# Kernel tuning notes

Measured on AMD Instinct MI355X. Metric: run time of the kernel, lower is better.

## Reference

```python
import jax, jax.numpy as jnp
import numpy as np

N_HEADS = 16
ROPE_BASE = 10000.0


def _rope(x):
    # x: (B, T, H, D) -> rotary position embedding, half-split style
    T, D = x.shape[1], x.shape[-1]
    inv_freq = 1.0 / (ROPE_BASE ** (jnp.arange(0, D, 2, dtype=jnp.float32) / D))  # (D/2,)
    ang = jnp.arange(T, dtype=jnp.float32)[:, None] * inv_freq[None, :]            # (T, D/2)
    cos = jnp.cos(ang)[None, :, None, :].astype(x.dtype)
    sin = jnp.sin(ang)[None, :, None, :].astype(x.dtype)
    x1, x2 = jnp.split(x, 2, axis=-1)
    return jnp.concatenate([x1 * cos - x2 * sin, x2 * cos + x1 * sin], axis=-1)


def setup_inputs() -> dict:
    key = jax.random.key(0)
    k1, k2, k3 = jax.random.split(key, 3)
    B, T, C = 4, 2048, 2048
    init_std = 0.02
    n_layers = 24  # n_text_layers + n_vision_layers
    x = jax.random.normal(k1, (B, T, C), dtype=jnp.float32)
    Wqkv = jax.random.normal(k2, (C, 3 * C), dtype=jnp.float32) * init_std
    Wproj = jax.random.normal(k3, (C, C), dtype=jnp.float32) * (init_std * 2 * n_layers ** (-0.5))
    return {"x": x, "Wqkv": Wqkv, "Wproj": Wproj}


def reference(x, Wqkv, Wproj):
    B, T, C = x.shape
    D = C // N_HEADS
    qkv = x @ Wqkv                                  # (B, T, 3C) fused QKV projection
    q, k, v = jnp.split(qkv, 3, axis=-1)
    q = q.reshape(B, T, N_HEADS, D)
    k = k.reshape(B, T, N_HEADS, D)
    v = v.reshape(B, T, N_HEADS, D)
    q = _rope(q)
    k = _rope(k)
    y = jax.nn.dot_product_attention(q, k, v, is_causal=True)  # (B, T, H, D)
    y = y.reshape(B, T, C)
    return y @ Wproj
```

## Files before the change

kernel.cpp:

```cpp
#include <hip/hip_runtime.h>

#define BB 4
#define TT 2048
#define CC 2048
#define NHEAD 16
#define DH 128
#define MM (BB * TT)
#define N3 (3 * CC)
#define LD3 6144

typedef unsigned short u16;
typedef __attribute__((ext_vector_type(8))) short short8;
typedef __attribute__((ext_vector_type(4))) float f32x4;

__device__ __forceinline__ u16 f2bf(float f) {
  unsigned u = __float_as_uint(f);
  u += 0x7fffu + ((u >> 16) & 1u);
  return (u16)(u >> 16);
}
__device__ __forceinline__ float bf2f(u16 h) {
  return __uint_as_float(((unsigned)h) << 16);
}

__device__ __forceinline__ void gload_lds16(const void* g, void* l) {
  __builtin_amdgcn_global_load_lds((const __attribute__((address_space(1))) void*)g,
                                   (__attribute__((address_space(3))) void*)l, 16, 0, 0);
}

__device__ __forceinline__ f32x4 mfma16(short8 a, short8 b, f32x4 c) {
  return __builtin_amdgcn_mfma_f32_16x16x32_bf16(a, b, c, 0, 0, 0);
}

__global__ void convert_x_kernel(const float* __restrict__ x, u16* __restrict__ xb) {
  const int total = (MM * CC) / 4;
  const float4* xv = (const float4*)x;
  ushort4* ov = (ushort4*)xb;
  for (int i = blockIdx.x * blockDim.x + threadIdx.x; i < total; i += gridDim.x * blockDim.x) {
    float4 v = xv[i];
    ushort4 o;
    o.x = f2bf(v.x); o.y = f2bf(v.y); o.z = f2bf(v.z); o.w = f2bf(v.w);
    ov[i] = o;
  }
}

__global__ void transpose_bf16_kernel(const float* __restrict__ W, u16* __restrict__ Wt,
                                      int rows, int cols) {
  __shared__ float tile[32][33];
  const int n0 = blockIdx.x * 32, k0 = blockIdx.y * 32;
  const int tx = threadIdx.x, ty = threadIdx.y;
  #pragma unroll
  for (int i = 0; i < 4; ++i)
    tile[ty + 8 * i][tx] = W[(size_t)(k0 + ty + 8 * i) * cols + n0 + tx];
  __syncthreads();
  #pragma unroll
  for (int i = 0; i < 4; ++i)
    Wt[(size_t)(n0 + ty + 8 * i) * rows + k0 + tx] = f2bf(tile[tx][ty + 8 * i]);
}

__global__ void rope_table_kernel(float2* __restrict__ tab) {
  int idx = blockIdx.x * 256 + threadIdx.x;
  int t = idx >> 6, f = idx & 63;
  float freq = expf(-0.14391156831f * (float)f);
  float ang = (float)t * freq;
  float s, c;
  sincosf(ang, &s, &c);
  tab[idx] = make_float2(c, s);
}

__global__ void rope_apply_kernel(u16* __restrict__ qkv, const float2* __restrict__ tab) {
  int idx = blockIdx.x * 256 + threadIdx.x;
  int f8 = idx & 7;
  int h = (idx >> 3) & 15;
  int m = (idx >> 7) & 8191;
  int which = idx >> 20;
  int t = m & (TT - 1);
  u16* p = qkv + (size_t)m * LD3 + which * CC + h * DH + f8 * 8;
  short8 v1 = *(const short8*)p;
  short8 v2 = *(const short8*)(p + 64);
  const float2* cs = &tab[(t << 6) + f8 * 8];
  const float scale = which ? 1.0f : 0.08838834764831845f;
  short8 o1, o2;
  #pragma unroll
  for (int j = 0; j < 8; ++j) {
    float2 c = cs[j];
    float x1 = bf2f((u16)v1[j]), x2 = bf2f((u16)v2[j]);
    o1[j] = (short)f2bf((x1 * c.x - x2 * c.y) * scale);
    o2[j] = (short)f2bf((x2 * c.x + x1 * c.y) * scale);
  }
  *(short8*)p = o1;
  *(short8*)(p + 64) = o2;
}

#define TILE_B 32768

__device__ __forceinline__ int swz47(int x) { return x ^ (((x >> 7) & 7) << 4); }

__device__ __forceinline__ void stage_chunk(const u16* __restrict__ src, int K, int k0,
                                            char* ldsTile, int kind, int wid, int lane) {
  #pragma unroll
  for (int c = 0; c < 2; ++c) {
    int x;
    if (kind < 2) {
      x = (kind ? 8192 : 0) + c * 16384 + wid * 1024 + lane * 16;
    } else {
      int wl = wid * 2 + c;
      x = ((kind == 3) ? 4096 : 0) + (wl >> 2) * 8192 + (wl & 3) * 1024 + lane * 16;
    }
    int l = swz47(x);
    int r = l >> 7;
    int ce = (l >> 1) & 63;
    gload_lds16(src + (size_t)r * K + k0 + ce, ldsTile + (x - lane * 16));
  }
}

__global__ __launch_bounds__(512, 2) void gemm_bt_256(const u16* __restrict__ A,
                                                      const u16* __restrict__ Bt,
                                                      void* __restrict__ Cout,
                                                      int K, int ldc, int out_bf16) {
  __shared__ __align__(16) char As[2][TILE_B];
  __shared__ __align__(16) char Bs[2][TILE_B];
  const int tid = threadIdx.x;
  const int wid = tid >> 6, lane = tid & 63;
  const int l15 = lane & 15, g = lane >> 4;
  const int wr = wid >> 2, wc = wid & 3;
  const int nwg = gridDim.x * gridDim.y;
  const int orig = blockIdx.y * gridDim.x + blockIdx.x;
  const int swz = (orig & 7) * (nwg >> 3) + (orig >> 3);
  const int bx = swz % gridDim.x, by = swz / gridDim.x;
  const int row0 = by * 256, col0 = bx * 256;

  const u16* Ab = A + (size_t)row0 * K;
  const u16* Bb = Bt + (size_t)col0 * K;

  f32x4 acc[8][4];
  #pragma unroll
  for (int m = 0; m < 8; ++m)
    #pragma unroll
    for (int n = 0; n < 4; ++n) acc[m][n] = (f32x4){0.f, 0.f, 0.f, 0.f};

  const int abase = (wr * 128 + l15) * 128 + g * 16;
  const int bbase = (wc * 64 + l15) * 128 + g * 16;

  stage_chunk(Ab, K, 0, As[0], 0, wid, lane);
  stage_chunk(Bb, K, 0, Bs[0], 2, wid, lane);
  stage_chunk(Bb, K, 0, Bs[0], 3, wid, lane);
  stage_chunk(Ab, K, 0, As[0], 1, wid, lane);
  asm volatile("s_waitcnt vmcnt(0)" ::: "memory");
  __builtin_amdgcn_s_barrier();

  const int nt = K >> 6;
  short8 a[4][2], blo[2][2], bhi[2][2];
  for (int kt = 0; kt < nt; ++kt) {
    const int cur = kt & 1, nx = cur ^ 1;
    const bool hn = (kt + 1) < nt;
    const int kn = (kt + 1) << 6;
    const char* At = As[cur];
    const char* Btl = Bs[cur];

    #pragma unroll
    for (int m = 0; m < 4; ++m)
      #pragma unroll
      for (int ks = 0; ks < 2; ++ks)
        a[m][ks] = *(const short8*)(At + swz47(abase + m * 2048 + ks * 64));
    #pragma unroll
    for (int n = 0; n < 2; ++n)
      #pragma unroll
      for (int ks = 0; ks < 2; ++ks)
        blo[n][ks] = *(const short8*)(Btl + swz47(bbase + n * 2048 + ks * 64));
    if (hn) stage_chunk(Ab, K, kn, As[nx], 0, wid, lane);
    __builtin_amdgcn_s_barrier();
    __builtin_amdgcn_s_setprio(1);
    #pragma unroll
    for (int m = 0; m < 4; ++m)
      #pragma unroll
      for (int n = 0; n < 2; ++n)
        #pragma unroll
        for (int ks = 0; ks < 2; ++ks)
          acc[m][n] = mfma16(a[m][ks], blo[n][ks], acc[m][n]);
    __builtin_amdgcn_s_setprio(0);
    if (hn) asm volatile("s_waitcnt vmcnt(4)" ::: "memory");
    else    asm volatile("s_waitcnt vmcnt(2)" ::: "memory");
    __builtin_amdgcn_s_barrier();

    #pragma unroll
    for (int n = 0; n < 2; ++n)
      #pragma unroll
      for (int ks = 0; ks < 2; ++ks)
        bhi[n][ks] = *(const short8*)(Btl + swz47(bbase + (n + 2) * 2048 + ks * 64));
    if (hn) stage_chunk(Bb, K, kn, Bs[nx], 2, wid, lane);
    __builtin_amdgcn_s_barrier();
    __builtin_amdgcn_s_setprio(1);
    #pragma unroll
    for (int m = 0; m < 4; ++m)
      #pragma unroll
      for (int n = 0; n < 2; ++n)
        #pragma unroll
        for (int ks = 0; ks < 2; ++ks)
          acc[m][n + 2] = mfma16(a[m][ks], bhi[n][ks], acc[m][n + 2]);
    __builtin_amdgcn_s_setprio(0);
    if (hn) asm volatile("s_waitcnt vmcnt(4)" ::: "memory");
    else    asm volatile("s_waitcnt vmcnt(0)" ::: "memory");
    __builtin_amdgcn_s_barrier();

    #pragma unroll
    for (int m = 0; m < 4; ++m)
      #pragma unroll
      for (int ks = 0; ks < 2; ++ks)
        a[m][ks] = *(const short8*)(At + swz47(abase + (m + 4) * 2048 + ks * 64));
    if (hn) stage_chunk(Bb, K, kn, Bs[nx], 3, wid, lane);
    __builtin_amdgcn_s_barrier();
    __builtin_amdgcn_s_setprio(1);
    #pragma unroll
    for (int m = 0; m < 4; ++m)
      #pragma unroll
      for (int n = 0; n < 2; ++n)
        #pragma unroll
        for (int ks = 0; ks < 2; ++ks)
          acc[m + 4][n] = mfma16(a[m][ks], blo[n][ks], acc[m + 4][n]);
    __builtin_amdgcn_s_setprio(0);
    if (hn) asm volatile("s_waitcnt vmcnt(4)" ::: "memory");
    __builtin_amdgcn_s_barrier();

    if (hn) stage_chunk(Ab, K, kn, As[nx], 1, wid, lane);
    __builtin_amdgcn_s_barrier();
    __builtin_amdgcn_s_setprio(1);
    #pragma unroll
    for (int m = 0; m < 4; ++m)
      #pragma unroll
      for (int n = 0; n < 2; ++n)
        #pragma unroll
        for (int ks = 0; ks < 2; ++ks)
          acc[m + 4][n + 2] = mfma16(a[m][ks], bhi[n][ks], acc[m + 4][n + 2]);
    __builtin_amdgcn_s_setprio(0);
    if (hn) asm volatile("s_waitcnt vmcnt(4)" ::: "memory");
    __builtin_amdgcn_s_barrier();
  }

  if (out_bf16) {
    u16* Cb = (u16*)Cout;
    #pragma unroll
    for (int m = 0; m < 8; ++m)
      #pragma unroll
      for (int n = 0; n < 4; ++n) {
        int row = row0 + wr * 128 + m * 16 + 4 * g;
        int col = col0 + wc * 64 + n * 16 + l15;
        #pragma unroll
        for (int j = 0; j < 4; ++j)
          Cb[(size_t)(row + j) * ldc + col] = f2bf(acc[m][n][j]);
      }
  } else {
    float* Cf = (float*)Cout;
    #pragma unroll
    for (int m = 0; m < 8; ++m)
      #pragma unroll
      for (int n = 0; n < 4; ++n) {
        int row = row0 + wr * 128 + m * 16 + 4 * g;
        int col = col0 + wc * 64 + n * 16 + l15;
        #pragma unroll
        for (int j = 0; j < 4; ++j)
          Cf[(size_t)(row + j) * ldc + col] = acc[m][n][j];
      }
  }
}

#define QBLK 128
#define KBLK 64
#define PADV 72

__global__ __launch_bounds__(256, 2) void attn_kernel(const u16* __restrict__ qkv,
                                                      u16* __restrict__ y) {
  __shared__ __align__(16) u16 Ks[2][KBLK * 128];
  __shared__ __align__(16) u16 Vt[2][DH * PADV];
  const int tid = threadIdx.x;
  const int wid = tid >> 6, lane = tid & 63;
  const int l15 = lane & 15, g = lane >> 4;
  const int b = blockIdx.y >> 4, h = blockIdx.y & 15;
  const size_t rb = (size_t)b * TT;
  const int vk0 = (tid & 15) * 4, vd0 = (tid >> 4) * 8;

  for (int half = 0; half < 2; ++half) {
    const int qt0 = (half ? (15 - (int)blockIdx.x) : (int)blockIdx.x) * QBLK;

    short8 qf[2][4];
    {
      const u16* qbase = qkv + (rb + qt0 + wid * 32 + l15) * LD3 + h * DH;
      #pragma unroll
      for (int f = 0; f < 2; ++f)
        #pragma unroll
        for (int kk = 0; kk < 4; ++kk)
          qf[f][kk] = *(const short8*)(qbase + f * 16 * LD3 + kk * 32 + g * 8);
    }

    {
      const u16* kbase = qkv + (rb)*LD3 + CC + h * DH;
      #pragma unroll
      for (int c = 0; c < 4; ++c) {
        int chunk = c * 256 + tid;
        int r = chunk >> 4, s = chunk & 15;
        gload_lds16(kbase + (size_t)r * LD3 + (size_t)((s ^ (r & 7)) * 8),
                    &Ks[0][(c * 256 + wid * 64) * 8]);
      }
      const u16* vg = qkv + (rb + vk0) * LD3 + 2 * CC + h * DH + vd0;
      short8 r0 = *(const short8*)vg;
      short8 r1 = *(const short8*)(vg + LD3);
      short8 r2 = *(const short8*)(vg + 2 * LD3);
      short8 r3 = *(const short8*)(vg + 3 * LD3);
      #pragma unroll
      for (int j = 0; j < 8; ++j) {
        ushort4 w;
        w.x = (u16)r0[j]; w.y = (u16)r1[j]; w.z = (u16)r2[j]; w.w = (u16)r3[j];
        *(ushort4*)&Vt[0][(vd0 + j) * PADV + vk0] = w;
      }
    }
    asm volatile("s_waitcnt vmcnt(0)" ::: "memory");
    __syncthreads();

    f32x4 o[2][8];
    float mrun[2][4], lrun[2][4];
    #pragma unroll
    for (int f = 0; f < 2; ++f) {
      #pragma unroll
      for (int nf = 0; nf < 8; ++nf) o[f][nf] = (f32x4){0.f, 0.f, 0.f, 0.f};
      #pragma unroll
      for (int j = 0; j < 4; ++j) { mrun[f][j] = -1e30f; lrun[f][j] = 0.f; }
    }

    const int nt = qt0 / KBLK + 2;
    for (int it = 0; it < nt; ++it) {
      const int cur = it & 1, nxt = cur ^ 1;
      const bool havenext = (it + 1) < nt;
      if (havenext) {
        const int kvn = (it + 1) * KBLK;
        const u16* kbase = qkv + (rb + kvn) * LD3 + CC + h * DH;
        #pragma unroll
        for (int c = 0; c < 4; ++c) {
          int chunk = c * 256 + tid;
          int r = chunk >> 4, s = chunk & 15;
          gload_lds16(kbase + (size_t)r * LD3 + (size_t)((s ^ (r & 7)) * 8),
                      &Ks[nxt][(c * 256 + wid * 64) * 8]);
        }
      }

      f32x4 s4[2][4];
      #pragma unroll
      for (int f = 0; f < 2; ++f)
        #pragma unroll
        for (int jf = 0; jf < 4; ++jf) s4[f][jf] = (f32x4){0.f, 0.f, 0.f, 0.f};
      #pragma unroll
      for (int jf = 0; jf < 4; ++jf) {
        int krow = jf * 16 + l15;
        #pragma unroll
        for (int kk = 0; kk < 4; ++kk) {
          short8 kf = *(const short8*)((const char*)Ks[cur] + krow * 256 +
                                       ((kk * 64 + g * 16) ^ ((l15 & 7) << 4)));
          s4[0][jf] = mfma16(qf[0][kk], kf, s4[0][jf]);
          s4[1][jf] = mfma16(qf[1][kk], kf, s4[1][jf]);
        }
      }
      if (it >= nt - 2) {
        const int kvb = it * KBLK - qt0;
        #pragma unroll
        for (int f = 0; f < 2; ++f)
          #pragma unroll
          for (int jf = 0; jf < 4; ++jf)
            #pragma unroll
            for (int j = 0; j < 4; ++j)
              if (kvb + jf * 16 + l15 > wid * 32 + f * 16 + 4 * g + j)
                s4[f][jf][j] = -1e30f;
      }
      {
        float rmax[2][4];
        #pragma unroll
        for (int f = 0; f < 2; ++f) {
          #pragma unroll
          for (int j = 0; j < 4; ++j)
            rmax[f][j] = fmaxf(fmaxf(s4[f][0][j], s4[f][1][j]),
                               fmaxf(s4[f][2][j], s4[f][3][j]));
          #pragma unroll
          for (int j = 0; j < 4; ++j) {
            rmax[f][j] = fmaxf(rmax[f][j], __shfl_xor(rmax[f][j], 1, 64));
            rmax[f][j] = fmaxf(rmax[f][j], __shfl_xor(rmax[f][j], 2, 64));
            rmax[f][j] = fmaxf(rmax[f][j], __shfl_xor(rmax[f][j], 4, 64));
            rmax[f][j] = fmaxf(rmax[f][j], __shfl_xor(rmax[f][j], 8, 64));
          }
        }
        bool small = true;
        #pragma unroll
        for (int f = 0; f < 2; ++f)
          #pragma unroll
          for (int j = 0; j < 4; ++j)
            small = small && (rmax[f][j] <= mrun[f][j] + 8.0f);
        if (!__all((int)small)) {
          #pragma unroll
          for (int f = 0; f < 2; ++f)
            #pragma unroll
            for (int j = 0; j < 4; ++j) {
              float mn = fmaxf(mrun[f][j], rmax[f][j]);
              float corr = __expf(mrun[f][j] - mn);
              mrun[f][j] = mn;
              lrun[f][j] *= corr;
              #pragma unroll
              for (int nf = 0; nf < 8; ++nf) o[f][nf][j] *= corr;
            }
        }
        #pragma unroll
        for (int f = 0; f < 2; ++f) {
          float rsum[4];
          #pragma unroll
          for (int jf = 0; jf < 4; ++jf)
            #pragma unroll
            for (int j = 0; j < 4; ++j)
              s4[f][jf][j] = __expf(s4[f][jf][j] - mrun[f][j]);
          #pragma unroll
          for (int j = 0; j < 4; ++j) {
            rsum[j] = (s4[f][0][j] + s4[f][1][j]) + (s4[f][2][j] + s4[f][3][j]);
            rsum[j] += __shfl_xor(rsum[j], 1, 64);
            rsum[j] += __shfl_xor(rsum[j], 2, 64);
            rsum[j] += __shfl_xor(rsum[j], 4, 64);
            rsum[j] += __shfl_xor(rsum[j], 8, 64);
            lrun[f][j] += rsum[j];
          }
        }
      }

      __syncthreads();
      {
        u16* Pb = (u16*)Ks[cur];
        #pragma unroll
        for (int f = 0; f < 2; ++f)
          #pragma unroll
          for (int jf = 0; jf < 4; ++jf)
            #pragma unroll
            for (int j = 0; j < 4; ++j) {
              int prow = wid * 32 + f * 16 + 4 * g + j;
              int pcol = (jf * 16 + l15) ^ (((4 * g + j) & 7) << 3);
              Pb[prow * 64 + pcol] = f2bf(s4[f][jf][j]);
            }
      }
      asm volatile("s_waitcnt lgkmcnt(0)" ::: "memory");
      __builtin_amdgcn_sched_barrier(0);
      short8 pf[2][2];
      #pragma unroll
      for (int f = 0; f < 2; ++f)
        #pragma unroll
        for (int kk = 0; kk < 2; ++kk)
          pf[f][kk] = *(const short8*)&((const u16*)Ks[cur])[
              (wid * 32 + f * 16 + l15) * 64 + ((kk * 32 + g * 8) ^ ((l15 & 7) << 3))];

      #pragma unroll
      for (int nf = 0; nf < 8; ++nf) {
        #pragma unroll
        for (int kk = 0; kk < 2; ++kk) {
          short8 vf = *(const short8*)&Vt[cur][(nf * 16 + l15) * PADV + kk * 32 + g * 8];
          o[0][nf] = mfma16(pf[0][kk], vf, o[0][nf]);
          o[1][nf] = mfma16(pf[1][kk], vf, o[1][nf]);
        }
      }

      if (havenext) {
        const int kvn = (it + 1) * KBLK;
        const u16* vg = qkv + (rb + kvn + vk0) * LD3 + 2 * CC + h * DH + vd0;
        short8 r0 = *(const short8*)vg;
        short8 r1 = *(const short8*)(vg + LD3);
        short8 r2 = *(const short8*)(vg + 2 * LD3);
        short8 r3 = *(const short8*)(vg + 3 * LD3);
        #pragma unroll
        for (int j = 0; j < 8; ++j) {
          ushort4 w;
          w.x = (u16)r0[j]; w.y = (u16)r1[j]; w.z = (u16)r2[j]; w.w = (u16)r3[j];
          *(ushort4*)&Vt[nxt][(vd0 + j) * PADV + vk0] = w;
        }
      }
      asm volatile("s_waitcnt vmcnt(0)" ::: "memory");
      __syncthreads();
    }

    #pragma unroll
    for (int f = 0; f < 2; ++f) {
      float inv[4];
      #pragma unroll
      for (int j = 0; j < 4; ++j) inv[j] = 1.0f / lrun[f][j];
      #pragma unroll
      for (int nf = 0; nf < 8; ++nf)
        #pragma unroll
        for (int j = 0; j < 4; ++j)
          y[(rb + qt0 + wid * 32 + f * 16 + 4 * g + j) * CC + h * DH + nf * 16 + l15] =
              f2bf(o[f][nf][j] * inv[j]);
    }
  }
}

extern "C" void kernel_launch(void* const* d_in, const int* in_sizes, int n_in,
                              void* d_out, int out_size, void* d_ws, size_t ws_size,
                              hipStream_t stream) {
  const float* x = (const float*)d_in[0];
  const float* Wqkv = (const float*)d_in[1];
  const float* Wproj = (const float*)d_in[2];
  char* ws = (char*)d_ws;
  u16* xb     = (u16*)(ws);
  u16* wqkvT  = (u16*)(ws + 33554432);
  u16* wprojT = (u16*)(ws + 58720256);
  u16* qkv    = (u16*)(ws + 67108864);
  u16* y      = (u16*)(ws + 167772160);
  float2* tab = (float2*)(ws + 201326592);

  convert_x_kernel<<<4096, 256, 0, stream>>>(x, xb);
  transpose_bf16_kernel<<<dim3(192, 64), dim3(32, 8), 0, stream>>>(Wqkv, wqkvT, CC, N3);
  transpose_bf16_kernel<<<dim3(64, 64), dim3(32, 8), 0, stream>>>(Wproj, wprojT, CC, CC);
  rope_table_kernel<<<512, 256, 0, stream>>>(tab);
  gemm_bt_256<<<dim3(24, 32), 512, 0, stream>>>(xb, wqkvT, (void*)qkv, CC, LD3, 1);
  rope_apply_kernel<<<8192, 256, 0, stream>>>(qkv, tab);
  attn_kernel<<<dim3(8, 64), 256, 0, stream>>>(qkv, y);
  gemm_bt_256<<<dim3(8, 32), 512, 0, stream>>>(y, wprojT, d_out, CC, CC, 0);
}
```

Baseline: 495.3 us.

## Fuse RoPE and query scaling into the QKV GEMM epilogue

Removes the separate rope_apply kernel and applies rotary embedding plus the query softmax scale directly in the QKV GEMM's bf16 store. To make this possible, the B-column assignment across waves is remapped so each wave holds both halves (d and d+64) of a head in registers. This saves a full read-modify-write pass over the Q and K parts of the qkv buffer. In exchange, the epilogue does per-element table lookups with strided scalar stores, and the changed column mapping may alter LDS access patterns.

Result: faster. 479.9 us (-3.1%).

```diff
diff --git a/kernel.cpp b/kernel.cpp
--- a/kernel.cpp
+++ b/kernel.cpp
@@ -67,30 +67,6 @@
   tab[idx] = make_float2(c, s);
 }
 
-__global__ void rope_apply_kernel(u16* __restrict__ qkv, const float2* __restrict__ tab) {
-  int idx = blockIdx.x * 256 + threadIdx.x;
-  int f8 = idx & 7;
-  int h = (idx >> 3) & 15;
-  int m = (idx >> 7) & 8191;
-  int which = idx >> 20;
-  int t = m & (TT - 1);
-  u16* p = qkv + (size_t)m * LD3 + which * CC + h * DH + f8 * 8;
-  short8 v1 = *(const short8*)p;
-  short8 v2 = *(const short8*)(p + 64);
-  const float2* cs = &tab[(t << 6) + f8 * 8];
-  const float scale = which ? 1.0f : 0.08838834764831845f;
-  short8 o1, o2;
-  #pragma unroll
-  for (int j = 0; j < 8; ++j) {
-    float2 c = cs[j];
-    float x1 = bf2f((u16)v1[j]), x2 = bf2f((u16)v2[j]);
-    o1[j] = (short)f2bf((x1 * c.x - x2 * c.y) * scale);
-    o2[j] = (short)f2bf((x2 * c.x + x1 * c.y) * scale);
-  }
-  *(short8*)p = o1;
-  *(short8*)(p + 64) = o2;
-}
-
 #define TILE_B 32768
 
 __device__ __forceinline__ int swz47(int x) { return x ^ (((x >> 7) & 7) << 4); }
@@ -116,7 +92,9 @@
 __global__ __launch_bounds__(512, 2) void gemm_bt_256(const u16* __restrict__ A,
                                                       const u16* __restrict__ Bt,
                                                       void* __restrict__ Cout,
-                                                      int K, int ldc, int out_bf16) {
+                                                      const float2* __restrict__ tab,
+                                                      int K, int ldc, int out_bf16,
+                                                      int rope_mode) {
   __shared__ __align__(16) char As[2][TILE_B];
   __shared__ __align__(16) char Bs[2][TILE_B];
   const int tid = threadIdx.x;
@@ -138,8 +116,12 @@
     #pragma unroll
     for (int n = 0; n < 4; ++n) acc[m][n] = (f32x4){0.f, 0.f, 0.f, 0.f};
 
+  int bcol[4];
+  #pragma unroll
+  for (int n = 0; n < 4; ++n)
+    bcol[n] = (wc & 1) * 32 + (wc >> 1) * 128 + ((n >> 1) << 6) + ((n & 1) << 4);
+
   const int abase = (wr * 128 + l15) * 128 + g * 16;
-  const int bbase = (wc * 64 + l15) * 128 + g * 16;
 
   stage_chunk(Ab, K, 0, As[0], 0, wid, lane);
   stage_chunk(Bb, K, 0, Bs[0], 2, wid, lane);
@@ -166,7 +148,8 @@
     for (int n = 0; n < 2; ++n)
       #pragma unroll
       for (int ks = 0; ks < 2; ++ks)
-        blo[n][ks] = *(const short8*)(Btl + swz47(bbase + n * 2048 + ks * 64));
+        blo[n][ks] = *(const short8*)(Btl +
+            swz47((bcol[n] + l15) * 128 + g * 16 + ks * 64));
     if (hn) stage_chunk(Ab, K, kn, As[nx], 0, wid, lane);
     __builtin_amdgcn_s_barrier();
     __builtin_amdgcn_s_setprio(1);
@@ -186,7 +169,8 @@
     for (int n = 0; n < 2; ++n)
       #pragma unroll
       for (int ks = 0; ks < 2; ++ks)
-        bhi[n][ks] = *(const short8*)(Btl + swz47(bbase + (n + 2) * 2048 + ks * 64));
+        bhi[n][ks] = *(const short8*)(Btl +
+            swz47((bcol[n + 2] + l15) * 128 + g * 16 + ks * 64));
     if (hn) stage_chunk(Bb, K, kn, Bs[nx], 2, wid, lane);
     __builtin_amdgcn_s_barrier();
     __builtin_amdgcn_s_setprio(1);
@@ -238,24 +222,46 @@
 
   if (out_bf16) {
     u16* Cb = (u16*)Cout;
+    if (rope_mode && col0 < 4096) {
+      const bool isq = (col0 < 2048);
+      const float qs = isq ? 0.08838834764831845f : 1.0f;
+      #pragma unroll
+      for (int m = 0; m < 8; ++m)
+        #pragma unroll
+        for (int n = 0; n < 2; ++n) {
+          int colL = col0 + bcol[n] + l15;
+          int f = (wc & 1) * 32 + ((n & 1) << 4) + l15;
+          #pragma unroll
+          for (int j = 0; j < 4; ++j) {
+            int row = row0 + wr * 128 + m * 16 + 4 * g + j;
+            float2 cs = tab[((row & (TT - 1)) << 6) + f];
+            float x1 = acc[m][n][j], x2 = acc[m][n + 2][j];
+            float o1 = (x1 * cs.x - x2 * cs.y) * qs;
+            float o2 = (x2 * cs.x + x1 * cs.y) * qs;
+            Cb[(size_t)row * ldc + colL] = f2bf(o1);
+            Cb[(size_t)row * ldc + colL + 64] = f2bf(o2);
+          }
+        }
+    } else {
+      #pragma unroll
+      for (int m = 0; m < 8; ++m)
+        #pragma unroll
+        for (int n = 0; n < 4; ++n) {
+          int row = row0 + wr * 128 + m * 16 + 4 * g;
+          int col = col0 + bcol[n] + l15;
+          #pragma unroll
+          for (int j = 0; j < 4; ++j)
+            Cb[(size_t)(row + j) * ldc + col] = f2bf(acc[m][n][j]);
+        }
+    }
+  } else {
+    float* Cf = (float*)Cout;
     #pragma unroll
     for (int m = 0; m < 8; ++m)
       #pragma unroll
       for (int n = 0; n < 4; ++n) {
         int row = row0 + wr * 128 + m * 16 + 4 * g;
-        int col = col0 + wc * 64 + n * 16 + l15;
-        #pragma unroll
-        for (int j = 0; j < 4; ++j)
-          Cb[(size_t)(row + j) * ldc + col] = f2bf(acc[m][n][j]);
-      }
-  } else {
-    float* Cf = (float*)Cout;
-    #pragma unroll
-    for (int m = 0; m < 8; ++m)
-      #pragma unroll
-      for (int n = 0; n < 4; ++n) {
-        int row = row0 + wr * 128 + m * 16 + 4 * g;
-        int col = col0 + wc * 64 + n * 16 + l15;
+        int col = col0 + bcol[n] + l15;
         #pragma unroll
         for (int j = 0; j < 4; ++j)
           Cf[(size_t)(row + j) * ldc + col] = acc[m][n][j];
@@ -508,8 +514,7 @@
   transpose_bf16_kernel<<<dim3(192, 64), dim3(32, 8), 0, stream>>>(Wqkv, wqkvT, CC, N3);
   transpose_bf16_kernel<<<dim3(64, 64), dim3(32, 8), 0, stream>>>(Wproj, wprojT, CC, CC);
   rope_table_kernel<<<512, 256, 0, stream>>>(tab);
-  gemm_bt_256<<<dim3(24, 32), 512, 0, stream>>>(xb, wqkvT, (void*)qkv, CC, LD3, 1);
-  rope_apply_kernel<<<8192, 256, 0, stream>>>(qkv, tab);
+  gemm_bt_256<<<dim3(24, 32), 512, 0, stream>>>(xb, wqkvT, (void*)qkv, tab, CC, LD3, 1, 1);
   attn_kernel<<<dim3(8, 64), 256, 0, stream>>>(qkv, y);
-  gemm_bt_256<<<dim3(8, 32), 512, 0, stream>>>(y, wprojT, d_out, CC, CC, 0);
-}
+  gemm_bt_256<<<dim3(8, 32), 512, 0, stream>>>(y, wprojT, d_out, tab, CC, CC, 0, 0);
+}
```
